# Kernel tuning notes

Hardware: AMD Instinct MI355X
Metric: run time of the kernel (lower is better)

The kernel has to match this reference:

```python
import jax, jax.numpy as jnp
import numpy as np

A = -0.75  # cv2 INTER_CUBIC cubic-convolution coefficient

def _cubic_kernel(d):
    d = jnp.abs(d)
    return jnp.where(
        d <= 1.0, (A + 2.0) * d**3 - (A + 3.0) * d**2 + 1.0,
        jnp.where(d < 2.0, A * d**3 - 5.0 * A * d**2 + 8.0 * A * d - 4.0 * A, 0.0))

def _resize_last_axis(x, s):
    # Bicubic upsample along the last axis by integer factor s (half-pixel
    # aligned, replicate border), matching cv2.resize INTER_CUBIC semantics.
    n = x.shape[-1]
    out_n = n * s
    src = (jnp.arange(out_n, dtype=jnp.float32) + 0.5) / s - 0.5
    base = jnp.floor(src).astype(jnp.int32)
    t = src - base.astype(jnp.float32)
    offs = jnp.arange(-1, 3)                      # 4 taps
    w = _cubic_kernel(t[:, None] - offs[None, :].astype(jnp.float32))  # [out_n,4]
    idx = jnp.clip(base[:, None] + offs[None, :], 0, n - 1)            # [out_n,4]
    g = x[..., idx]                                # [..., out_n, 4]
    return jnp.einsum('...ok,ok->...o', g, w)

def bicubic_upscale(x, s):
    # x: [B,C,H,W] -> [B,C,H*s,W*s], separable bicubic
    y = _resize_last_axis(x, s)                    # along W
    y = jnp.swapaxes(y, -1, -2)
    y = _resize_last_axis(y, s)                    # along H
    return jnp.swapaxes(y, -1, -2)

def _conv(x, w, b, pad):
    y = jax.lax.conv_general_dilated(
        x, w, window_strides=(1, 1), padding=[(pad, pad), (pad, pad)],
        dimension_numbers=('NCHW', 'OIHW', 'NCHW'))
    return y + b[None, :, None, None]

def setup_inputs() -> dict:
    key = jax.random.key(0)
    ks = jax.random.split(key, 4)
    x = jax.random.normal(ks[0], (16, 32, 32, 4), dtype=jnp.float32)
    w1 = jax.random.normal(ks[1], (64, 4, 9, 9), dtype=jnp.float32) * (1.0 / np.sqrt(4 * 81))
    b1 = jnp.zeros((64,), jnp.float32)
    w2 = jax.random.normal(ks[2], (32, 64, 1, 1), dtype=jnp.float32) * (1.0 / np.sqrt(64))
    b2 = jnp.zeros((32,), jnp.float32)
    w3 = jax.random.normal(ks[3], (4, 32, 5, 5), dtype=jnp.float32) * (1.0 / np.sqrt(32 * 25))
    b3 = jnp.zeros((4,), jnp.float32)
    return {"x": x, "w1": w1, "b1": b1, "w2": w2, "b2": b2, "w3": w3, "b3": b3}

def reference(x, w1, b1, w2, b2, w3, b3):
    xc = jnp.transpose(x, (0, 3, 1, 2))            # NHWC -> NCHW
    up = bicubic_upscale(xc, 8)                    # [B,4,256,256]
    h = jax.nn.relu(_conv(up, w1, b1, 4))          # 9x9, 4->64
    h = jax.nn.relu(_conv(h, w2, b2, 0))           # 1x1, 64->32
    out = _conv(h, w3, b3, 2)                      # 5x5, 32->4
    return jnp.transpose(out, (0, 2, 3, 1))        # NCHW -> NHWC
```

## Files before the change

kernel.cpp:

```cpp
#include <hip/hip_runtime.h>
#include <hip/hip_bf16.h>

typedef unsigned short ushort_t;
typedef __attribute__((ext_vector_type(8))) short v8s;
typedef __attribute__((ext_vector_type(4))) float v4f;

#define B1F_F   33792
#define B2F_F   33856
#define B3F_F   33888
#define WTAB_F  33892
#define FLAG_I  33924
#define PK1_US  0
#define PK2_US  22528
#define PK3_US  26624
#define UP_US   69632
#define H2_US   4263936
#define CVT_TOTAL (22528 + 4096 + 40960 + 132)

__device__ __forceinline__ ushort_t f2us(float v) {
  __hip_bfloat16 h = __float2bfloat16(v);
  return *reinterpret_cast<ushort_t*>(&h);
}
__device__ __forceinline__ float us2f(unsigned int u) { return __uint_as_float(u << 16); }

__device__ __forceinline__ float load_in(const void* p, int i, int isbf16) {
  if (isbf16) return us2f(((const unsigned short*)p)[i]);
  return ((const float*)p)[i];
}
__device__ __forceinline__ float4 load_in4(const void* p, int i4, int isbf16) {
  if (isbf16) {
    unsigned long long q = *(const unsigned long long*)((const unsigned short*)p + i4);
    return make_float4(us2f((unsigned int)(q & 0xffff)),
                       us2f((unsigned int)((q >> 16) & 0xffff)),
                       us2f((unsigned int)((q >> 32) & 0xffff)),
                       us2f((unsigned int)((q >> 48) & 0xffff)));
  }
  return *(const float4*)((const float*)p + i4);
}

__device__ __forceinline__ float cubicw(float d) {
  const float Ac = -0.75f;
  d = fabsf(d);
  float d2 = d * d, d3 = d2 * d;
  if (d <= 1.f) return (Ac + 2.f) * d3 - (Ac + 3.f) * d2 + 1.f;
  if (d < 2.f)  return Ac * d3 - 5.f * Ac * d2 + 8.f * Ac * d - 4.f * Ac;
  return 0.f;
}

__global__ __launch_bounds__(256) void k_probe(const unsigned short* __restrict__ xr,
                                               int* __restrict__ flag) {
  __shared__ int s[256];
  int tid = threadIdx.x;
  int cnt = 0;
  for (int i = tid; i < 512; i += 256) {
    unsigned short h = xr[2 * i];
    int e = (h >> 7) & 0xFF;
    if (e >= 110 && e <= 135) cnt++;
  }
  s[tid] = cnt;
  __syncthreads();
  if (tid == 0) {
    int t = 0;
    for (int i = 0; i < 256; i++) t += s[i];
    flag[0] = (t >= 256) ? 1 : 0;
  }
}

__global__ __launch_bounds__(256) void k_cvt(
    const void* __restrict__ w1, const void* __restrict__ b1,
    const void* __restrict__ w2, const void* __restrict__ b2,
    const void* __restrict__ w3, const void* __restrict__ b3,
    ushort_t* __restrict__ wsus, float* __restrict__ wsf,
    const int* __restrict__ flag) {
  int i = blockIdx.x * 256 + threadIdx.x;
  if (i >= CVT_TOTAL) return;
  const int f = flag[0];
  if (i < 22528) {
    int j  = i & 7;
    int l  = (i >> 3) & 63;
    int nt = (i >> 9) & 3;
    int ks = i >> 11;
    int k  = ks * 32 + ((l >> 4) & 3) * 8 + j;
    int oc = nt * 16 + (l & 15);
    float v = 0.f;
    if (k < 324) {
      int tap = k >> 2, ic = k & 3;
      int ky = tap / 9, kx = tap - ky * 9;
      v = load_in(w1, ((oc * 4 + ic) * 9 + ky) * 9 + kx, f);
    }
    wsus[PK1_US + i] = f2us(v);
    return;
  }
  if (i < 26624) {
    int t = i - 22528;
    int j  = t & 7;
    int l  = (t >> 3) & 63;
    int nt = (t >> 9) & 1;
    int ks = (t >> 10) & 1;
    int part = t >> 11;
    int oc1 = ks * 32 + ((l >> 4) & 3) * 8 + j;
    int oc2 = nt * 16 + (l & 15);
    float w = load_in(w2, oc2 * 64 + oc1, f);
    float hi = us2f(f2us(w));
    wsus[PK2_US + t] = part ? f2us(w - hi) : f2us(w);
    return;
  }
  if (i < 67584) {
    int t = i - 26624;
    int part = t / 20480;
    int r = t - part * 20480;
    int j8 = r & 7;
    int l  = (r >> 3) & 63;
    int ks = r >> 9;
    int k  = ks * 32 + ((l >> 4) & 3) * 8 + j8;
    int n  = l & 15;
    int ky = k >> 8, jj = (k >> 5) & 7, ic = k & 31;
    int dx = n >> 2, oc = n & 3;
    int kx = jj - dx;
    float w = 0.f;
    if (kx >= 0 && kx <= 4)
      w = load_in(w3, ((oc * 32 + ic) * 5 + ky) * 5 + kx, f);
    float hi = us2f(f2us(w));
    wsus[PK3_US + t] = part ? f2us(w - hi) : f2us(w);
    return;
  }
  int t = i - 67584;
  if (t < 64) { wsf[B1F_F + t] = load_in(b1, t, f); return; }
  if (t < 96) { wsf[B2F_F + (t - 64)] = load_in(b2, t - 64, f); return; }
  if (t < 100) { wsf[B3F_F + (t - 96)] = load_in(b3, t - 96, f); return; }
  if (t < 132) {
    int p = (t - 100) >> 2, a = (t - 100) & 3;
    float frac = (p + 0.5f) * 0.125f - 0.5f;
    float fl = floorf(frac);
    float tt = frac - fl;
    wsf[WTAB_F + (t - 100)] = cubicw(tt - (float)(a - 1));
  }
}

__global__ __launch_bounds__(256) void k_upscale(
    const void* __restrict__ x, ushort_t* __restrict__ up,
    const float* __restrict__ wsf, const int* __restrict__ flag) {
  const int f = flag[0];
  int n = blockIdx.x * 256 + threadIdx.x;
  int xo = n & 255, yo = (n >> 8) & 255, b = n >> 16;
  int px = xo & 7, py = yo & 7;
  const float* wt = wsf + WTAB_F;
  float4 wx = *(const float4*)(wt + px * 4);
  float4 wy = *(const float4*)(wt + py * 4);
  float wya[4] = {wy.x, wy.y, wy.z, wy.w};
  int bx = (xo >> 3) + ((px >= 4) ? 0 : -1);
  int by = (yo >> 3) + ((py >= 4) ? 0 : -1);
  int ix0 = min(max(bx - 1, 0), 31), ix1 = min(max(bx, 0), 31);
  int ix2 = min(max(bx + 1, 0), 31), ix3 = min(max(bx + 2, 0), 31);
  float ax = 0.f, ay = 0.f, az = 0.f, aw = 0.f;
#pragma unroll
  for (int a = 0; a < 4; a++) {
    int iy = min(max(by + a - 1, 0), 31);
    int rowb = (b * 32 + iy) * 32;
    float4 p0 = load_in4(x, (rowb + ix0) * 4, f);
    float4 p1 = load_in4(x, (rowb + ix1) * 4, f);
    float4 p2 = load_in4(x, (rowb + ix2) * 4, f);
    float4 p3 = load_in4(x, (rowb + ix3) * 4, f);
    float rx = wx.x * p0.x + wx.y * p1.x + wx.z * p2.x + wx.w * p3.x;
    float ry = wx.x * p0.y + wx.y * p1.y + wx.z * p2.y + wx.w * p3.y;
    float rz = wx.x * p0.z + wx.y * p1.z + wx.z * p2.z + wx.w * p3.z;
    float rw = wx.x * p0.w + wx.y * p1.w + wx.z * p2.w + wx.w * p3.w;
    ax = fmaf(wya[a], rx, ax); ay = fmaf(wya[a], ry, ay);
    az = fmaf(wya[a], rz, az); aw = fmaf(wya[a], rw, aw);
  }
  unsigned long long q =
      (unsigned long long)f2us(ax) |
      ((unsigned long long)f2us(ay) << 16) |
      ((unsigned long long)f2us(az) << 32) |
      ((unsigned long long)f2us(aw) << 48);
  *(unsigned long long*)(up + n * 4) = q;
}

__global__ __launch_bounds__(256) void k_conv12(
    const ushort_t* __restrict__ up, const ushort_t* __restrict__ wsus,
    const float* __restrict__ wsf, ushort_t* __restrict__ h2) {
  __shared__ __align__(16) ushort_t patchA[16 * 48 * 4];
  __shared__ __align__(16) ushort_t h1[256 * 72];
  const int b  = blockIdx.z;
  const int x0 = blockIdx.x * 32, y0 = blockIdx.y * 8;
  const int tid = threadIdx.x;

#pragma unroll
  for (int i = 0; i < 3; ++i) {
    int e = tid + i * 256;
    int yy = e / 48, xx = e % 48;
    int gy = y0 + yy - 4, gx = x0 + xx - 4;
    unsigned long long q = 0ull;
    if (gy >= 0 && gy < 256 && gx >= 0 && gx < 256)
      q = *(const unsigned long long*)(up + (((b * 256 + gy) * 256 + gx) << 2));
    *(unsigned long long*)(patchA + e * 4) = q;
  }
  __syncthreads();

  const int lane = tid & 63, wave = tid >> 6;
  const int quad = lane >> 4, lc = lane & 15;
  int base_m[4], pix0_[4];
#pragma unroll
  for (int i = 0; i < 4; ++i) {
    int mt = wave * 4 + i;
    int py = mt >> 1, pxh = (mt & 1) << 4;
    base_m[i] = (py * 48 + pxh + lc) << 2;
    pix0_[i] = py * 32 + pxh;
  }
  v4f acc[4][4];
#pragma unroll
  for (int i = 0; i < 4; ++i)
#pragma unroll
    for (int nt = 0; nt < 4; ++nt) acc[i][nt] = (v4f){0.f, 0.f, 0.f, 0.f};

  const v8s* __restrict__ Bp = (const v8s*)(wsus + PK1_US);
  for (int ks = 0; ks < 11; ++ks) {
    v8s Bf[4];
#pragma unroll
    for (int nt = 0; nt < 4; ++nt) Bf[nt] = Bp[(ks * 4 + nt) * 64 + lane];
    int tap0 = ks * 8 + quad * 2;
    int tap1 = min(tap0 + 1, 80);
    tap0 = min(tap0, 80);
    int ky0 = tap0 / 9, kx0 = tap0 - ky0 * 9;
    int ky1 = tap1 / 9, kx1 = tap1 - ky1 * 9;
    int off0 = (ky0 * 48 + kx0) << 2;
    int off1 = (ky1 * 48 + kx1) << 2;
#pragma unroll
    for (int i = 0; i < 4; ++i) {
      union { unsigned long long q[2]; v8s v; } u;
      u.q[0] = *(const unsigned long long*)(patchA + base_m[i] + off0);
      u.q[1] = *(const unsigned long long*)(patchA + base_m[i] + off1);
#pragma unroll
      for (int nt = 0; nt < 4; ++nt)
        acc[i][nt] = __builtin_amdgcn_mfma_f32_16x16x32_bf16(u.v, Bf[nt], acc[i][nt], 0, 0, 0);
    }
  }

  float b1v[4];
#pragma unroll
  for (int nt = 0; nt < 4; ++nt) b1v[nt] = (wsf + B1F_F)[nt * 16 + lc];
#pragma unroll
  for (int i = 0; i < 4; ++i) {
#pragma unroll
    for (int nt = 0; nt < 4; ++nt) {
#pragma unroll
      for (int r = 0; r < 4; ++r) {
        int pix = pix0_[i] + (quad << 2) + r;
        float vv = fmaxf(acc[i][nt][r] + b1v[nt], 0.f);
        h1[pix * 72 + nt * 16 + lc] = f2us(vv);
      }
    }
  }

  v4f acc2[4][2];
#pragma unroll
  for (int i = 0; i < 4; ++i) { acc2[i][0] = (v4f){0,0,0,0}; acc2[i][1] = (v4f){0,0,0,0}; }
  const v8s* __restrict__ Bp2 = (const v8s*)(wsus + PK2_US);
#pragma unroll
  for (int ks = 0; ks < 2; ++ks) {
    v8s af[4];
#pragma unroll
    for (int i = 0; i < 4; ++i)
      af[i] = *(const v8s*)(h1 + (pix0_[i] + lc) * 72 + ks * 32 + quad * 8);
#pragma unroll
    for (int part = 0; part < 2; ++part) {
#pragma unroll
      for (int nt = 0; nt < 2; ++nt) {
        v8s Bf = Bp2[((part * 2 + ks) * 2 + nt) * 64 + lane];
#pragma unroll
        for (int i = 0; i < 4; ++i)
          acc2[i][nt] = __builtin_amdgcn_mfma_f32_16x16x32_bf16(af[i], Bf, acc2[i][nt], 0, 0, 0);
      }
    }
  }

  float b2v[2];
  b2v[0] = (wsf + B2F_F)[lc];
  b2v[1] = (wsf + B2F_F)[16 + lc];
#pragma unroll
  for (int i = 0; i < 4; ++i) {
#pragma unroll
    for (int nt = 0; nt < 2; ++nt) {
#pragma unroll
      for (int r = 0; r < 4; ++r) {
        int pix = pix0_[i] + (quad << 2) + r;
        int gy = y0 + (pix >> 5), gx = x0 + (pix & 31);
        float vv = fmaxf(acc2[i][nt][r] + b2v[nt], 0.f);
        h2[(((b * 256 + gy) * 256 + gx) << 5) + nt * 16 + lc] = f2us(vv);
      }
    }
  }
}

__global__ __launch_bounds__(256) void k_conv3(
    const ushort_t* __restrict__ h2, const ushort_t* __restrict__ wsus,
    const float* __restrict__ wsf, void* __restrict__ out,
    const int* __restrict__ flag) {
  __shared__ __align__(16) ushort_t patch[20 * 1160];
  const int b  = blockIdx.z;
  const int x0 = blockIdx.x * 32, y0 = blockIdx.y * 16;
  const int tid = threadIdx.x;

  for (int e = tid; e < 720; e += 256) {
    int yy = e / 36, xx = e - yy * 36;
    int gy = y0 + yy - 2, gx = x0 + xx - 2;
    ushort_t* dst = patch + yy * 1160 + xx * 32;
    if (gy >= 0 && gy < 256 && gx >= 0 && gx < 256) {
      const ushort_t* src = h2 + (((b * 256 + gy) * 256 + gx) << 5);
#pragma unroll
      for (int c = 0; c < 4; ++c)
        *(float4*)(dst + c * 8) = *(const float4*)(src + c * 8);
    } else {
      float4 z = make_float4(0.f, 0.f, 0.f, 0.f);
#pragma unroll
      for (int c = 0; c < 4; ++c) *(float4*)(dst + c * 8) = z;
    }
  }
  __syncthreads();

  const int lane = tid & 63, wave = tid >> 6;
  const int quad = lane >> 4, lc = lane & 15;
  v4f acc[2];
  acc[0] = (v4f){0.f, 0.f, 0.f, 0.f};
  acc[1] = (v4f){0.f, 0.f, 0.f, 0.f};
  const v8s* __restrict__ Bp3 = (const v8s*)(wsus + PK3_US);

  for (int ks = 0; ks < 40; ++ks) {
    v8s Bh = Bp3[ks * 64 + lane];
    v8s Bl = Bp3[(40 + ks) * 64 + lane];
    int ky = ks >> 3, j = ks & 7;
    int rowoff = (lc + ky) * 1160 + j * 32 + quad * 8;
#pragma unroll
    for (int i = 0; i < 2; ++i) {
      int q = wave * 2 + i;
      v8s Af = *(const v8s*)(patch + rowoff + q * 128);
      acc[i] = __builtin_amdgcn_mfma_f32_16x16x32_bf16(Af, Bh, acc[i], 0, 0, 0);
      acc[i] = __builtin_amdgcn_mfma_f32_16x16x32_bf16(Af, Bl, acc[i], 0, 0, 0);
    }
  }

  float b3v = (wsf + B3F_F)[lc & 3];
  const int fl = flag[0];
#pragma unroll
  for (int i = 0; i < 2; ++i) {
    int q = wave * 2 + i;
#pragma unroll
    for (int r = 0; r < 4; ++r) {
      int gy = y0 + (quad << 2) + r;
      int gx = x0 + (q << 2) + (lc >> 2);
      int idx = (((b * 256 + gy) * 256 + gx) << 2) + (lc & 3);
      float vv = acc[i][r] + b3v;
      if (fl) ((ushort_t*)out)[idx] = f2us(vv);
      else    ((float*)out)[idx] = vv;
    }
  }
}

extern "C" void kernel_launch(void* const* d_in, const int* in_sizes, int n_in,
                              void* d_out, int out_size, void* d_ws, size_t ws_size,
                              hipStream_t stream) {
  const void* x  = d_in[0];
  const void* w1 = d_in[1];
  const void* b1 = d_in[2];
  const void* w2 = d_in[3];
  const void* b2 = d_in[4];
  const void* w3 = d_in[5];
  const void* b3 = d_in[6];

  ushort_t* wsus = (ushort_t*)d_ws;
  float* wsf = (float*)d_ws;
  int* flag = (int*)((float*)d_ws + FLAG_I);
  ushort_t* up = wsus + UP_US;
  ushort_t* h2 = wsus + H2_US;

  k_probe<<<1, 256, 0, stream>>>((const unsigned short*)x, flag);
  k_cvt<<<(CVT_TOTAL + 255) / 256, 256, 0, stream>>>(w1, b1, w2, b2, w3, b3, wsus, wsf, flag);
  k_upscale<<<4096, 256, 0, stream>>>(x, up, wsf, flag);
  k_conv12<<<dim3(8, 32, 16), 256, 0, stream>>>(up, wsus, wsf, h2);
  k_conv3<<<dim3(8, 16, 16), 256, 0, stream>>>(h2, wsus, wsf, d_out, flag);
}
```

Measured before the change: 180.0 us.

## Fuse 1x1 conv in registers, drop split-bf16 conv3 pass, merge probe into cvt

The 9x9 conv now computes the transposed product (weights as A, pixels as B), so its accumulator layout can be fed straight into the 1x1 conv MFMA from registers. This removes the LDS h1 buffer and its round trip, and the 1x1 weights stay in registers. The conv3 low-part (hi/lo bf16 split) MFMA pass is dropped, halving its matrix work at some cost in accuracy. The dtype probe kernel is folded into the weight-conversion kernel, removing one launch, and bf16 packing uses a paired bit-trick rounding helper.

```diff
diff --git a/kernel.cpp b/kernel.cpp
--- a/kernel.cpp
+++ b/kernel.cpp
@@ -5,23 +5,30 @@
 typedef __attribute__((ext_vector_type(8))) short v8s;
 typedef __attribute__((ext_vector_type(4))) float v4f;
 
-#define B1F_F   33792
-#define B2F_F   33856
-#define B3F_F   33888
-#define WTAB_F  33892
-#define FLAG_I  33924
+#define B1F_F   23552
+#define B2F_F   23616
+#define B3F_F   23648
+#define WTAB_F  23652
+#define FLAG_I  23684
 #define PK1_US  0
 #define PK2_US  22528
 #define PK3_US  26624
-#define UP_US   69632
-#define H2_US   4263936
-#define CVT_TOTAL (22528 + 4096 + 40960 + 132)
+#define UP_US   48256
+#define H2_US   4242560
+#define CVT_TOTAL (47104 + 132)
 
 __device__ __forceinline__ ushort_t f2us(float v) {
   __hip_bfloat16 h = __float2bfloat16(v);
   return *reinterpret_cast<ushort_t*>(&h);
 }
 __device__ __forceinline__ float us2f(unsigned int u) { return __uint_as_float(u << 16); }
+
+__device__ __forceinline__ unsigned int bfpair(float a, float b) {
+  unsigned int ua = __float_as_uint(a), ub = __float_as_uint(b);
+  ua += 0x7fffu + ((ua >> 16) & 1u);
+  ub += 0x7fffu + ((ub >> 16) & 1u);
+  return (ua >> 16) | (ub & 0xffff0000u);
+}
 
 __device__ __forceinline__ float load_in(const void* p, int i, int isbf16) {
   if (isbf16) return us2f(((const unsigned short*)p)[i]);
@@ -47,34 +54,33 @@
   return 0.f;
 }
 
-__global__ __launch_bounds__(256) void k_probe(const unsigned short* __restrict__ xr,
-                                               int* __restrict__ flag) {
-  __shared__ int s[256];
-  int tid = threadIdx.x;
-  int cnt = 0;
-  for (int i = tid; i < 512; i += 256) {
-    unsigned short h = xr[2 * i];
-    int e = (h >> 7) & 0xFF;
-    if (e >= 110 && e <= 135) cnt++;
-  }
-  s[tid] = cnt;
-  __syncthreads();
-  if (tid == 0) {
-    int t = 0;
-    for (int i = 0; i < 256; i++) t += s[i];
-    flag[0] = (t >= 256) ? 1 : 0;
-  }
-}
-
 __global__ __launch_bounds__(256) void k_cvt(
+    const void* __restrict__ x,
     const void* __restrict__ w1, const void* __restrict__ b1,
     const void* __restrict__ w2, const void* __restrict__ b2,
     const void* __restrict__ w3, const void* __restrict__ b3,
     ushort_t* __restrict__ wsus, float* __restrict__ wsf,
-    const int* __restrict__ flag) {
-  int i = blockIdx.x * 256 + threadIdx.x;
+    int* __restrict__ flag) {
+  __shared__ int scnt;
+  const int tid = threadIdx.x;
+  if (tid == 0) scnt = 0;
+  __syncthreads();
+  {
+    const unsigned short* xr = (const unsigned short*)x;
+    int c = 0;
+    for (int s = tid; s < 512; s += 256) {
+      unsigned short h = xr[2 * s];
+      int e = (h >> 7) & 0xFF;
+      if (e >= 110 && e <= 135) c++;
+    }
+    if (c) atomicAdd(&scnt, c);
+  }
+  __syncthreads();
+  const int f = (scnt >= 256) ? 1 : 0;
+  if (blockIdx.x == 0 && tid == 0) flag[0] = f;
+
+  int i = blockIdx.x * 256 + tid;
   if (i >= CVT_TOTAL) return;
-  const int f = flag[0];
   if (i < 22528) {
     int j  = i & 7;
     int l  = (i >> 3) & 63;
@@ -93,25 +99,22 @@
   }
   if (i < 26624) {
     int t = i - 22528;
-    int j  = t & 7;
-    int l  = (t >> 3) & 63;
-    int nt = (t >> 9) & 1;
-    int ks = (t >> 10) & 1;
-    int part = t >> 11;
-    int oc1 = ks * 32 + ((l >> 4) & 3) * 8 + j;
-    int oc2 = nt * 16 + (l & 15);
+    int j   = t & 7;
+    int l   = (t >> 3) & 63;
+    int mt2 = (t >> 9) & 1;
+    int nt  = (t >> 10) & 3;
+    int oc1 = nt * 16 + ((l >> 4) & 3) * 4 + (j & 3);
+    int oc2 = mt2 * 16 + (l & 15);
     float w = load_in(w2, oc2 * 64 + oc1, f);
     float hi = us2f(f2us(w));
-    wsus[PK2_US + t] = part ? f2us(w - hi) : f2us(w);
+    wsus[PK2_US + t] = (j < 4) ? f2us(w) : f2us(w - hi);
     return;
   }
-  if (i < 67584) {
+  if (i < 47104) {
     int t = i - 26624;
-    int part = t / 20480;
-    int r = t - part * 20480;
-    int j8 = r & 7;
-    int l  = (r >> 3) & 63;
-    int ks = r >> 9;
+    int j8 = t & 7;
+    int l  = (t >> 3) & 63;
+    int ks = t >> 9;
     int k  = ks * 32 + ((l >> 4) & 3) * 8 + j8;
     int n  = l & 15;
     int ky = k >> 8, jj = (k >> 5) & 7, ic = k & 31;
@@ -120,11 +123,10 @@
     float w = 0.f;
     if (kx >= 0 && kx <= 4)
       w = load_in(w3, ((oc * 32 + ic) * 5 + ky) * 5 + kx, f);
-    float hi = us2f(f2us(w));
-    wsus[PK3_US + t] = part ? f2us(w - hi) : f2us(w);
+    wsus[PK3_US + t] = f2us(w);
     return;
   }
-  int t = i - 67584;
+  int t = i - 47104;
   if (t < 64) { wsf[B1F_F + t] = load_in(b1, t, f); return; }
   if (t < 96) { wsf[B2F_F + (t - 64)] = load_in(b2, t - 64, f); return; }
   if (t < 100) { wsf[B3F_F + (t - 96)] = load_in(b3, t - 96, f); return; }
@@ -169,10 +171,8 @@
     az = fmaf(wya[a], rz, az); aw = fmaf(wya[a], rw, aw);
   }
   unsigned long long q =
-      (unsigned long long)f2us(ax) |
-      ((unsigned long long)f2us(ay) << 16) |
-      ((unsigned long long)f2us(az) << 32) |
-      ((unsigned long long)f2us(aw) << 48);
+      (unsigned long long)bfpair(ax, ay) |
+      ((unsigned long long)bfpair(az, aw) << 32);
   *(unsigned long long*)(up + n * 4) = q;
 }
 
@@ -180,7 +180,6 @@
     const ushort_t* __restrict__ up, const ushort_t* __restrict__ wsus,
     const float* __restrict__ wsf, ushort_t* __restrict__ h2) {
   __shared__ __align__(16) ushort_t patchA[16 * 48 * 4];
-  __shared__ __align__(16) ushort_t h1[256 * 72];
   const int b  = blockIdx.z;
   const int x0 = blockIdx.x * 32, y0 = blockIdx.y * 8;
   const int tid = threadIdx.x;
@@ -213,11 +212,18 @@
 #pragma unroll
     for (int nt = 0; nt < 4; ++nt) acc[i][nt] = (v4f){0.f, 0.f, 0.f, 0.f};
 
-  const v8s* __restrict__ Bp = (const v8s*)(wsus + PK1_US);
+  v8s w2f[4][2];
+#pragma unroll
+  for (int nt = 0; nt < 4; ++nt)
+#pragma unroll
+    for (int mt2 = 0; mt2 < 2; ++mt2)
+      w2f[nt][mt2] = ((const v8s*)(wsus + PK2_US))[(nt * 2 + mt2) * 64 + lane];
+
+  const v8s* __restrict__ Ap1 = (const v8s*)(wsus + PK1_US);
   for (int ks = 0; ks < 11; ++ks) {
-    v8s Bf[4];
-#pragma unroll
-    for (int nt = 0; nt < 4; ++nt) Bf[nt] = Bp[(ks * 4 + nt) * 64 + lane];
+    v8s Af[4];
+#pragma unroll
+    for (int nt = 0; nt < 4; ++nt) Af[nt] = Ap1[(ks * 4 + nt) * 64 + lane];
     int tap0 = ks * 8 + quad * 2;
     int tap1 = min(tap0 + 1, 80);
     tap0 = min(tap0, 80);
@@ -232,62 +238,50 @@
       u.q[1] = *(const unsigned long long*)(patchA + base_m[i] + off1);
 #pragma unroll
       for (int nt = 0; nt < 4; ++nt)
-        acc[i][nt] = __builtin_amdgcn_mfma_f32_16x16x32_bf16(u.v, Bf[nt], acc[i][nt], 0, 0, 0);
-    }
-  }
-
-  float b1v[4];
-#pragma unroll
-  for (int nt = 0; nt < 4; ++nt) b1v[nt] = (wsf + B1F_F)[nt * 16 + lc];
+        acc[i][nt] = __builtin_amdgcn_mfma_f32_16x16x32_bf16(Af[nt], u.v, acc[i][nt], 0, 0, 0);
+    }
+  }
+
+  float4 b1q[4];
+#pragma unroll
+  for (int nt = 0; nt < 4; ++nt)
+    b1q[nt] = *(const float4*)(wsf + B1F_F + nt * 16 + quad * 4);
+  float4 b2q[2];
+#pragma unroll
+  for (int mt2 = 0; mt2 < 2; ++mt2)
+    b2q[mt2] = *(const float4*)(wsf + B2F_F + mt2 * 16 + quad * 4);
+
 #pragma unroll
   for (int i = 0; i < 4; ++i) {
+    v4f a2[2];
+    a2[0] = (v4f){0.f, 0.f, 0.f, 0.f};
+    a2[1] = (v4f){0.f, 0.f, 0.f, 0.f};
 #pragma unroll
     for (int nt = 0; nt < 4; ++nt) {
-#pragma unroll
-      for (int r = 0; r < 4; ++r) {
-        int pix = pix0_[i] + (quad << 2) + r;
-        float vv = fmaxf(acc[i][nt][r] + b1v[nt], 0.f);
-        h1[pix * 72 + nt * 16 + lc] = f2us(vv);
-      }
-    }
-  }
-
-  v4f acc2[4][2];
-#pragma unroll
-  for (int i = 0; i < 4; ++i) { acc2[i][0] = (v4f){0,0,0,0}; acc2[i][1] = (v4f){0,0,0,0}; }
-  const v8s* __restrict__ Bp2 = (const v8s*)(wsus + PK2_US);
-#pragma unroll
-  for (int ks = 0; ks < 2; ++ks) {
-    v8s af[4];
-#pragma unroll
-    for (int i = 0; i < 4; ++i)
-      af[i] = *(const v8s*)(h1 + (pix0_[i] + lc) * 72 + ks * 32 + quad * 8);
-#pragma unroll
-    for (int part = 0; part < 2; ++part) {
-#pragma unroll
-      for (int nt = 0; nt < 2; ++nt) {
-        v8s Bf = Bp2[((part * 2 + ks) * 2 + nt) * 64 + lane];
-#pragma unroll
-        for (int i = 0; i < 4; ++i)
-          acc2[i][nt] = __builtin_amdgcn_mfma_f32_16x16x32_bf16(af[i], Bf, acc2[i][nt], 0, 0, 0);
-      }
-    }
-  }
-
-  float b2v[2];
-  b2v[0] = (wsf + B2F_F)[lc];
-  b2v[1] = (wsf + B2F_F)[16 + lc];
-#pragma unroll
-  for (int i = 0; i < 4; ++i) {
-#pragma unroll
-    for (int nt = 0; nt < 2; ++nt) {
-#pragma unroll
-      for (int r = 0; r < 4; ++r) {
-        int pix = pix0_[i] + (quad << 2) + r;
-        int gy = y0 + (pix >> 5), gx = x0 + (pix & 31);
-        float vv = fmaxf(acc2[i][nt][r] + b2v[nt], 0.f);
-        h2[(((b * 256 + gy) * 256 + gx) << 5) + nt * 16 + lc] = f2us(vv);
-      }
+      float r0 = fmaxf(acc[i][nt][0] + b1q[nt].x, 0.f);
+      float r1 = fmaxf(acc[i][nt][1] + b1q[nt].y, 0.f);
+      float r2 = fmaxf(acc[i][nt][2] + b1q[nt].z, 0.f);
+      float r3 = fmaxf(acc[i][nt][3] + b1q[nt].w, 0.f);
+      unsigned int u0 = bfpair(r0, r1), u1 = bfpair(r2, r3);
+      union { unsigned int q[4]; v8s v; } bu;
+      bu.q[0] = u0; bu.q[1] = u1; bu.q[2] = u0; bu.q[3] = u1;
+#pragma unroll
+      for (int mt2 = 0; mt2 < 2; ++mt2)
+        a2[mt2] = __builtin_amdgcn_mfma_f32_16x16x32_bf16(w2f[nt][mt2], bu.v, a2[mt2], 0, 0, 0);
+    }
+    int pix = pix0_[i] + lc;
+    int gy = y0 + (pix >> 5), gx = x0 + (pix & 31);
+    ushort_t* dst = h2 + (((b * 256 + gy) * 256 + gx) << 5) + (quad << 2);
+#pragma unroll
+    for (int mt2 = 0; mt2 < 2; ++mt2) {
+      float v0 = fmaxf(a2[mt2][0] + b2q[mt2].x, 0.f);
+      float v1 = fmaxf(a2[mt2][1] + b2q[mt2].y, 0.f);
+      float v2 = fmaxf(a2[mt2][2] + b2q[mt2].z, 0.f);
+      float v3 = fmaxf(a2[mt2][3] + b2q[mt2].w, 0.f);
+      unsigned long long q =
+          (unsigned long long)bfpair(v0, v1) |
+          ((unsigned long long)bfpair(v2, v3) << 32);
+      *(unsigned long long*)(dst + mt2 * 16) = q;
     }
   }
 }
@@ -327,7 +321,6 @@
 
   for (int ks = 0; ks < 40; ++ks) {
     v8s Bh = Bp3[ks * 64 + lane];
-    v8s Bl = Bp3[(40 + ks) * 64 + lane];
     int ky = ks >> 3, j = ks & 7;
     int rowoff = (lc + ky) * 1160 + j * 32 + quad * 8;
 #pragma unroll
@@ -335,7 +328,6 @@
       int q = wave * 2 + i;
       v8s Af = *(const v8s*)(patch + rowoff + q * 128);
       acc[i] = __builtin_amdgcn_mfma_f32_16x16x32_bf16(Af, Bh, acc[i], 0, 0, 0);
-      acc[i] = __builtin_amdgcn_mfma_f32_16x16x32_bf16(Af, Bl, acc[i], 0, 0, 0);
     }
   }
 
@@ -373,8 +365,8 @@
   ushort_t* up = wsus + UP_US;
   ushort_t* h2 = wsus + H2_US;
 
-  k_probe<<<1, 256, 0, stream>>>((const unsigned short*)x, flag);
-  k_cvt<<<(CVT_TOTAL + 255) / 256, 256, 0, stream>>>(w1, b1, w2, b2, w3, b3, wsus, wsf, flag);
+  k_cvt<<<(CVT_TOTAL + 255) / 256, 256, 0, stream>>>(x, w1, b1, w2, b2, w3, b3,
+                                                     wsus, wsf, flag);
   k_upscale<<<4096, 256, 0, stream>>>(x, up, wsf, flag);
   k_conv12<<<dim3(8, 32, 16), 256, 0, stream>>>(up, wsus, wsf, h2);
   k_conv3<<<dim3(8, 16, 16), 256, 0, stream>>>(h2, wsus, wsf, d_out, flag);
```

Result: faster. 171.0 us (-5.0%).
